# Performance work log

Measured on AMD Instinct MI355X. Metric: run time of the kernel, lower is better.

## Reference

```python
import jax, jax.numpy as jnp
import numpy as np

EPS = 1e-5

def conv_bn(x, w, bn):
    # 1x1 conv (no bias) + BatchNorm2d in eval mode.
    # x: [B,C,H,W], w: [O,C], bn: [4,O] = (gamma, beta, running_mean, running_var)
    y = jnp.einsum('bchw,oc->bohw', x, w)
    g, b, m, v = bn[0], bn[1], bn[2], bn[3]
    s = g * jax.lax.rsqrt(v + EPS)
    return y * s[None, :, None, None] + (b - m * s)[None, :, None, None]

def setup_inputs() -> dict:
    key = jax.random.key(0)
    ks = jax.random.split(key, 10)
    dim, nh_kd, dh = 384, 256, 1024
    return {
        'x':   jax.random.normal(ks[0], (16, dim, 32, 32), dtype=jnp.float32),
        'wq':  jax.random.normal(ks[1], (nh_kd, dim), dtype=jnp.float32) * 0.05,
        'bnq': jax.random.uniform(ks[2], (4, nh_kd), dtype=jnp.float32),
        'wk':  jax.random.normal(ks[3], (nh_kd, dim), dtype=jnp.float32) * 0.05,
        'bnk': jax.random.uniform(ks[4], (4, nh_kd), dtype=jnp.float32),
        'wv':  jax.random.normal(ks[5], (dh, dim), dtype=jnp.float32) * 0.05,
        'bnv': jax.random.uniform(ks[6], (4, dh), dtype=jnp.float32),
        'wp':  jax.random.normal(ks[7], (dim, dh), dtype=jnp.float32) * 0.05,
        'bnp': jax.random.uniform(ks[8], (4, dim), dtype=jnp.float32),
        'num_heads': 8,
    }

def reference(x, wq, bnq, wk, bnk, wv, bnv, wp, bnp, num_heads):
    B, C, H, W = x.shape
    N = H * W
    nh = num_heads
    kd = wq.shape[0] // nh          # key_dim
    d = wv.shape[0] // nh           # attn_ratio * key_dim
    dh = wv.shape[0]
    scale = kd ** (-0.5)

    qq = conv_bn(x, wq, bnq).reshape(B, nh, kd, N).transpose(0, 1, 3, 2)  # [B,nh,N,kd]
    kk = conv_bn(x, wk, bnk).reshape(B, nh, kd, N)                         # [B,nh,kd,N]
    vv = conv_bn(x, wv, bnv).reshape(B, nh, d, N).transpose(0, 1, 3, 2)    # [B,nh,N,d]

    # NOTE: original divides by scale (i.e. multiplies by sqrt(key_dim)); kept faithfully.
    attn = jnp.einsum('bhnk,bhkm->bhnm', qq, kk) / scale
    attn = jax.nn.softmax(attn, axis=-1)
    xx = jnp.einsum('bhnm,bhmd->bhnd', attn, vv)           # [B,nh,N,d]
    xx = xx.transpose(0, 1, 3, 2).reshape(B, dh, H, W)
    return conv_bn(xx, wp, bnp)
```

## Files before the change

### kernel.cpp

```cpp
#include <hip/hip_runtime.h>

typedef _Float16 f16x8 __attribute__((ext_vector_type(8)));
typedef _Float16 f16x4 __attribute__((ext_vector_type(4)));
typedef __fp16 h16x2 __attribute__((ext_vector_type(2)));
typedef float f32x4 __attribute__((ext_vector_type(4)));
typedef float f32x16 __attribute__((ext_vector_type(16)));

#define BN_EPS 1e-5f
#define SQRT32 5.656854249492381f
#define LOG2E  1.4426950408889634f

typedef const __attribute__((address_space(1))) void* gas_p;
typedef __attribute__((address_space(3))) void* las_p;

__global__ __launch_bounds__(256) void prep(
    const float* __restrict__ x,
    const float* __restrict__ wq, const float* __restrict__ wk,
    const float* __restrict__ wv, const float* __restrict__ wp,
    const float* __restrict__ bnq, const float* __restrict__ bnk,
    const float* __restrict__ bnv, const float* __restrict__ bnp,
    _Float16* __restrict__ xT_hi, _Float16* __restrict__ xT_lo,
    _Float16* __restrict__ wqk_h, _Float16* __restrict__ wqk_l,
    _Float16* __restrict__ wv_h,  _Float16* __restrict__ wp_h,
    float* __restrict__ s_qkv, float* __restrict__ t_qkv,
    float* __restrict__ s_p,   float* __restrict__ t_p)
{
    __shared__ float Tx[64][65];
    const int t = threadIdx.x;
    if (blockIdx.z < 16) {
        const int ct = blockIdx.x, nt = blockIdx.y, b = blockIdx.z;
        const int c0 = ct * 64, n0 = nt * 64;
        {
            int tr = t >> 4, tc = (t & 15) * 4;
            #pragma unroll
            for (int p = 0; p < 4; p++) {
                int r = tr + p * 16;
                float4 v = *(const float4*)(x + ((size_t)(b * 384 + c0 + r)) * 1024 + n0 + tc);
                Tx[r][tc + 0] = v.x; Tx[r][tc + 1] = v.y; Tx[r][tc + 2] = v.z; Tx[r][tc + 3] = v.w;
            }
        }
        __syncthreads();
        {
            int nn = t >> 2, cc = (t & 3) * 16;
            f16x8 h0, h1, l0, l1;
            #pragma unroll
            for (int i = 0; i < 8; i++) {
                float v = Tx[cc + i][nn];
                _Float16 hh = (_Float16)v;
                h0[i] = hh; l0[i] = (_Float16)(v - (float)hh);
            }
            #pragma unroll
            for (int i = 0; i < 8; i++) {
                float v = Tx[cc + 8 + i][nn];
                _Float16 hh = (_Float16)v;
                h1[i] = hh; l1[i] = (_Float16)(v - (float)hh);
            }
            size_t o = ((size_t)(b * 1024 + n0 + nn)) * 384 + c0 + cc;
            *(f16x8*)(xT_hi + o) = h0; *(f16x8*)(xT_hi + o + 8) = h1;
            *(f16x8*)(xT_lo + o) = l0; *(f16x8*)(xT_lo + o + 8) = l1;
        }
    } else {
        const int NQK = 512 * 384, NV = 1024 * 384, NP = 384 * 1024;
        int tid = (blockIdx.y * 6 + blockIdx.x) * 256 + t;
        for (int i = tid; i < NQK + NV + NP; i += 24576) {
            if (i < NQK) {
                int o = i / 384, c = i - o * 384;
                float v = (o < 256) ? wq[o * 384 + c] : wk[(o - 256) * 384 + c];
                _Float16 hh = (_Float16)v;
                wqk_h[i] = hh; wqk_l[i] = (_Float16)(v - (float)hh);
            } else if (i < NQK + NV) {
                wv_h[i - NQK] = (_Float16)wv[i - NQK];
            } else {
                wp_h[i - NQK - NV] = (_Float16)wp[i - NQK - NV];
            }
        }
        if (tid < 1536) {
            int i = tid;
            float g, be, m, v;
            if (i < 256)      { int o = i;       g = bnq[o]; be = bnq[256 + o];  m = bnq[512 + o];  v = bnq[768 + o]; }
            else if (i < 512) { int o = i - 256; g = bnk[o]; be = bnk[256 + o];  m = bnk[512 + o];  v = bnk[768 + o]; }
            else              { int o = i - 512; g = bnv[o]; be = bnv[1024 + o]; m = bnv[2048 + o]; v = bnv[3072 + o]; }
            float s = g * rsqrtf(v + BN_EPS);
            float tt = be - m * s;
            if (i < 256) { s *= SQRT32 * LOG2E; tt *= SQRT32 * LOG2E; }
            s_qkv[i] = s; t_qkv[i] = tt;
        } else if (tid < 1536 + 384) {
            int o = tid - 1536;
            float g = bnp[o], be = bnp[384 + o], m = bnp[768 + o], v = bnp[1152 + o];
            float s = g * rsqrtf(v + BN_EPS);
            s_p[o] = s; t_p[o] = be - m * s;
        }
    }
}

__global__ __launch_bounds__(256, 2) void gemm_qkv(
    const _Float16* __restrict__ wqk_h, const _Float16* __restrict__ wqk_l,
    const _Float16* __restrict__ wv_h,
    const _Float16* __restrict__ xT_hi, const _Float16* __restrict__ xT_lo,
    const float* __restrict__ S, const float* __restrict__ T,
    _Float16* __restrict__ qT_h, _Float16* __restrict__ qT_l,
    _Float16* __restrict__ kT_h, _Float16* __restrict__ kT_l,
    _Float16* __restrict__ vbuf)
{
    __shared__ __align__(16) _Float16 As_h[128 * 40];
    __shared__ __align__(16) _Float16 As_l[128 * 40];
    __shared__ __align__(16) _Float16 Bs_h[128 * 40];
    __shared__ __align__(16) _Float16 Bs_l[128 * 40];
    const int t = threadIdx.x, lane = t & 63, w = t >> 6;
    const int wr = w >> 1, wc = w & 1, l16 = lane & 15, lq = lane >> 4;
    const int bx = blockIdx.x, n0 = blockIdx.y * 128, b = blockIdx.z;
    const bool isv = bx >= 4;
    const int o0 = isv ? (bx - 4) * 128 : bx * 128;
    const _Float16* __restrict__ Ah = isv ? wv_h : wqk_h;

    f32x4 acc[4][4] = {};

    for (int kb = 0; kb < 384; kb += 32) {
        __syncthreads();
        #pragma unroll
        for (int p = 0; p < 2; p++) {
            int g = t + p * 256, row = g >> 2, ch = g & 3;
            *(uint4*)(&As_h[row * 40 + ch * 8]) =
                *(const uint4*)(Ah + (size_t)(o0 + row) * 384 + kb + ch * 8);
        }
        #pragma unroll
        for (int p = 0; p < 2; p++) {
            int g = t + p * 256, row = g >> 2, ch = g & 3;
            *(uint4*)(&Bs_h[row * 40 + ch * 8]) =
                *(const uint4*)(xT_hi + ((size_t)(b * 1024) + n0 + row) * 384 + kb + ch * 8);
        }
        if (!isv) {
            #pragma unroll
            for (int p = 0; p < 2; p++) {
                int g = t + p * 256, row = g >> 2, ch = g & 3;
                *(uint4*)(&As_l[row * 40 + ch * 8]) =
                    *(const uint4*)(wqk_l + (size_t)(o0 + row) * 384 + kb + ch * 8);
            }
            #pragma unroll
            for (int p = 0; p < 2; p++) {
                int g = t + p * 256, row = g >> 2, ch = g & 3;
                *(uint4*)(&Bs_l[row * 40 + ch * 8]) =
                    *(const uint4*)(xT_lo + ((size_t)(b * 1024) + n0 + row) * 384 + kb + ch * 8);
            }
        }
        __syncthreads();

        if (!isv) {
            f16x8 ah[4], al[4], bh[4], bl[4];
            #pragma unroll
            for (int i = 0; i < 4; i++) {
                ah[i] = *(const f16x8*)(&Bs_h[(wr * 64 + i * 16 + l16) * 40 + lq * 8]);
                al[i] = *(const f16x8*)(&Bs_l[(wr * 64 + i * 16 + l16) * 40 + lq * 8]);
            }
            #pragma unroll
            for (int j = 0; j < 4; j++) {
                bh[j] = *(const f16x8*)(&As_h[(wc * 64 + j * 16 + l16) * 40 + lq * 8]);
                bl[j] = *(const f16x8*)(&As_l[(wc * 64 + j * 16 + l16) * 40 + lq * 8]);
            }
            #pragma unroll
            for (int i = 0; i < 4; i++)
                #pragma unroll
                for (int j = 0; j < 4; j++) {
                    acc[i][j] = __builtin_amdgcn_mfma_f32_16x16x32_f16(ah[i], bh[j], acc[i][j], 0, 0, 0);
                    acc[i][j] = __builtin_amdgcn_mfma_f32_16x16x32_f16(al[i], bh[j], acc[i][j], 0, 0, 0);
                    acc[i][j] = __builtin_amdgcn_mfma_f32_16x16x32_f16(ah[i], bl[j], acc[i][j], 0, 0, 0);
                }
        } else {
            f16x8 a[4], bf[4];
            #pragma unroll
            for (int i = 0; i < 4; i++) a[i]  = *(const f16x8*)(&As_h[(wr * 64 + i * 16 + l16) * 40 + lq * 8]);
            #pragma unroll
            for (int j = 0; j < 4; j++) bf[j] = *(const f16x8*)(&Bs_h[(wc * 64 + j * 16 + l16) * 40 + lq * 8]);
            #pragma unroll
            for (int i = 0; i < 4; i++)
                #pragma unroll
                for (int j = 0; j < 4; j++)
                    acc[i][j] = __builtin_amdgcn_mfma_f32_16x16x32_f16(a[i], bf[j], acc[i][j], 0, 0, 0);
        }
    }

    if (!isv) {
        #pragma unroll
        for (int i = 0; i < 4; i++) {
            #pragma unroll
            for (int r = 0; r < 4; r++) {
                int n = n0 + wr * 64 + i * 16 + lq * 4 + r;
                #pragma unroll
                for (int j = 0; j < 4; j++) {
                    int o = o0 + wc * 64 + j * 16 + l16;
                    float sc = S[o], sh = T[o];
                    float v = acc[i][j][r] * sc + sh;
                    _Float16 hh = (_Float16)v;
                    _Float16 ll = (_Float16)(v - (float)hh);
                    if (o < 256) {
                        size_t idx = (((size_t)(b * 8) + (o >> 5)) * 1024 + n) * 32 + (o & 31);
                        qT_h[idx] = hh; qT_l[idx] = ll;
                    } else {
                        int oo = o - 256;
                        int hd = oo >> 5, c = oo & 31;
                        int f = ((n >> 5) & 1) * 2 + (c >> 4);
                        size_t idx = ((((size_t)(b * 8 + hd) * 16 + (n >> 6)) * 4 + f) * 64
                                      + ((c >> 3) & 1) * 32 + (n & 31)) * 8 + (c & 7);
                        kT_h[idx] = hh; kT_l[idx] = ll;
                    }
                }
            }
        }
    } else {
        #pragma unroll
        for (int i = 0; i < 4; i++) {
            #pragma unroll
            for (int r = 0; r < 4; r++) {
                int o = o0 + wr * 64 + i * 16 + lq * 4 + r;
                float sc = S[512 + o], sh = T[512 + o];
                #pragma unroll
                for (int j = 0; j < 4; j++) {
                    int n = n0 + wc * 64 + j * 16 + l16;
                    int k = n & 63;
                    int s4 = k >> 4, c4 = (k >> 2) & 3;
                    int ep = s4 * 16 + (c4 & 1) * 8 + (c4 >> 1) * 4 + (k & 3);
                    int nst = (n & ~63) | ep;
                    vbuf[((size_t)(b * 1024) + o) * 1024 + nst] = (_Float16)(acc[i][j][r] * sc + sh);
                }
            }
        }
    }
}

__device__ __forceinline__ f32x16 qk6(f16x8 kh0, f16x8 kl0, f16x8 kh1, f16x8 kl1,
                                      f16x8 qh0, f16x8 ql0, f16x8 qh1, f16x8 ql1) {
    f32x16 c = {};
    c = __builtin_amdgcn_mfma_f32_32x32x16_f16(kh0, qh0, c, 0, 0, 0);
    c = __builtin_amdgcn_mfma_f32_32x32x16_f16(kl0, qh0, c, 0, 0, 0);
    c = __builtin_amdgcn_mfma_f32_32x32x16_f16(kh0, ql0, c, 0, 0, 0);
    c = __builtin_amdgcn_mfma_f32_32x32x16_f16(kh1, qh1, c, 0, 0, 0);
    c = __builtin_amdgcn_mfma_f32_32x32x16_f16(kl1, qh1, c, 0, 0, 0);
    c = __builtin_amdgcn_mfma_f32_32x32x16_f16(kh1, ql1, c, 0, 0, 0);
    return c;
}

__global__ __launch_bounds__(256, 3) void attn(
    const _Float16* __restrict__ qT_h, const _Float16* __restrict__ qT_l,
    const _Float16* __restrict__ kT_h, const _Float16* __restrict__ kT_l,
    const _Float16* __restrict__ vbuf,
    _Float16* __restrict__ xxT_h, _Float16* __restrict__ xxT_l)
{
    __shared__ __align__(16) _Float16 Vs[2][128 * 64];
    __shared__ __align__(16) _Float16 Ksh[2][2048];
    __shared__ __align__(16) _Float16 Ksl[2][2048];
    const int t = threadIdx.x, lane = t & 63, w = t >> 6;
    const int L = lane & 31, hl = lane >> 5;
    const int bh = blockIdx.x, qt = blockIdx.y;
    const int b = bh >> 3, h = bh & 7;
    const size_t vbase = ((size_t)(b * 1024) + h * 128) * 1024;

    f16x8 bq_h[2], bq_l[2];
    {
        int q = qt * 128 + w * 32 + L;
        #pragma unroll
        for (int kh = 0; kh < 2; kh++) {
            size_t base = ((size_t)(bh * 1024) + q) * 32 + kh * 16 + hl * 8;
            bq_h[kh] = *(const f16x8*)(qT_h + base);
            bq_l[kh] = *(const f16x8*)(qT_l + base);
        }
    }

    f32x16 o_acc[4] = {};
    float m_st = -INFINITY, l_st = 0.f;

    #define DMA_TILE(buf, kt_)                                                     \
        {                                                                          \
            size_t ktb = (size_t)(bh * 16 + (kt_)) * 2048 + (size_t)t * 8;         \
            __builtin_amdgcn_global_load_lds((gas_p)(const void*)(kT_h + ktb),     \
                                             (las_p)(void*)&Ksh[buf][w * 512], 16, 0, 0); \
            __builtin_amdgcn_global_load_lds((gas_p)(const void*)(kT_l + ktb),     \
                                             (las_p)(void*)&Ksl[buf][w * 512], 16, 0, 0); \
            _Pragma("unroll")                                                      \
            for (int p = 0; p < 4; p++) {                                          \
                int g2 = t + p * 256;                                              \
                int d = g2 >> 3;                                                   \
                int kcg = (g2 & 7) ^ (d & 7);                                      \
                const _Float16* src = vbuf + vbase + (size_t)d * 1024              \
                                      + (kt_) * 64 + kcg * 8;                      \
                _Float16* dst = &Vs[buf][(p * 256 + w * 64) * 8];                  \
                __builtin_amdgcn_global_load_lds((gas_p)(const void*)src,          \
                                                 (las_p)(void*)dst, 16, 0, 0);     \
            }                                                                      \
        }

    DMA_TILE(0, 0)
    __syncthreads();

    for (int kt = 0; kt < 16; kt++) {
        const int cur = kt & 1;

        if (kt < 15) DMA_TILE(cur ^ 1, kt + 1)

        const _Float16* khp = &Ksh[cur][lane * 8];
        const _Float16* klp = &Ksl[cur][lane * 8];
        f16x8 K0h = *(const f16x8*)(khp);
        f16x8 K1h = *(const f16x8*)(khp + 512);
        f16x8 K2h = *(const f16x8*)(khp + 1024);
        f16x8 K3h = *(const f16x8*)(khp + 1536);
        f16x8 K0l = *(const f16x8*)(klp);
        f16x8 K1l = *(const f16x8*)(klp + 512);
        f16x8 K2l = *(const f16x8*)(klp + 1024);
        f16x8 K3l = *(const f16x8*)(klp + 1536);

        __builtin_amdgcn_s_setprio(1);
        f32x16 c0 = qk6(K0h, K0l, K1h, K1l, bq_h[0], bq_l[0], bq_h[1], bq_l[1]);
        f32x16 c1 = qk6(K2h, K2l, K3h, K3l, bq_h[0], bq_l[0], bq_h[1], bq_l[1]);
        __builtin_amdgcn_s_setprio(0);

        float tmx[16];
        #pragma unroll
        for (int i = 0; i < 16; i++) tmx[i] = fmaxf(c0[i], c1[i]);
        #pragma unroll
        for (int st = 8; st >= 1; st >>= 1)
            #pragma unroll
            for (int i = 0; i < st; i++) tmx[i] = fmaxf(tmx[i], tmx[i + st]);
        float mx = fmaxf(tmx[0], __shfl_xor(tmx[0], 32, 64));

        if (__any(mx > m_st + 8.f)) {
            float mnew = fmaxf(m_st, mx);
            float a = exp2f(m_st - mnew);
            l_st *= a;
            #pragma unroll
            for (int dt = 0; dt < 4; dt++)
                #pragma unroll
                for (int i = 0; i < 16; i++) o_acc[dt][i] *= a;
            m_st = mnew;
        }

        f16x8 pf[4];
        float rs = 0.f;
        #pragma unroll
        for (int s = 0; s < 4; s++) {
            float pv[8];
            #pragma unroll
            for (int j = 0; j < 8; j++) {
                float cv = (s < 2) ? c0[(s & 1) * 8 + j] : c1[(s & 1) * 8 + j];
                pv[j] = exp2f(cv - m_st);
            }
            rs += ((pv[0] + pv[1]) + (pv[2] + pv[3])) + ((pv[4] + pv[5]) + (pv[6] + pv[7]));
            union { f16x8 v; h16x2 h[4]; } u;
            #pragma unroll
            for (int j = 0; j < 4; j++)
                u.h[j] = __builtin_amdgcn_cvt_pkrtz(pv[2 * j], pv[2 * j + 1]);
            pf[s] = u.v;
        }
        l_st += rs;

        __builtin_amdgcn_s_setprio(1);
        #pragma unroll
        for (int s = 0; s < 4; s++) {
            #pragma unroll
            for (int dt = 0; dt < 4; dt++) {
                int cp = (2 * s + hl) ^ (L & 7);
                f16x8 avp = *(const f16x8*)(&Vs[cur][(dt * 32 + L) * 64 + cp * 8]);
                o_acc[dt] = __builtin_amdgcn_mfma_f32_32x32x16_f16(avp, pf[s], o_acc[dt], 0, 0, 0);
            }
        }
        __builtin_amdgcn_s_setprio(0);

        if (kt < 15) __syncthreads();
    }
    #undef DMA_TILE

    l_st += __shfl_xor(l_st, 32, 64);

    {
        float rl = 1.f / l_st;
        int q = qt * 128 + w * 32 + L;
        #pragma unroll
        for (int dt = 0; dt < 4; dt++) {
            #pragma unroll
            for (int gg = 0; gg < 4; gg++) {
                f16x4 hv, lv;
                #pragma unroll
                for (int rr = 0; rr < 4; rr++) {
                    float v = o_acc[dt][gg * 4 + rr] * rl;
                    _Float16 hh = (_Float16)v;
                    hv[rr] = hh; lv[rr] = (_Float16)(v - (float)hh);
                }
                size_t o = ((size_t)(b * 1024) + q) * 1024 + h * 128 + dt * 32 + gg * 8 + hl * 4;
                *(f16x4*)(xxT_h + o) = hv;
                *(f16x4*)(xxT_l + o) = lv;
            }
        }
    }
}

__global__ __launch_bounds__(256, 2) void gemm_out(
    const _Float16* __restrict__ wp_h,
    const _Float16* __restrict__ xxT_h, const _Float16* __restrict__ xxT_l,
    const float* __restrict__ S, const float* __restrict__ T,
    float* __restrict__ out)
{
    __shared__ __align__(16) _Float16 As[128 * 40];
    __shared__ __align__(16) _Float16 Bh[64 * 40];
    __shared__ __align__(16) _Float16 Bl[64 * 40];
    const int t = threadIdx.x, lane = t & 63, w = t >> 6;
    const int wr = w >> 1, wc = w & 1, l16 = lane & 15, lq = lane >> 4;
    const int o0 = blockIdx.x * 128, n0 = blockIdx.y * 64, b = blockIdx.z;

    f32x4 acc[4][2] = {};

    for (int kb = 0; kb < 1024; kb += 32) {
        __syncthreads();
        #pragma unroll
        for (int p = 0; p < 2; p++) {
            int g = t + p * 256, row = g >> 2, ch = g & 3;
            *(uint4*)(&As[row * 40 + ch * 8]) =
                *(const uint4*)(wp_h + (size_t)(o0 + row) * 1024 + kb + ch * 8);
        }
        {
            int row = t >> 2, ch = t & 3;
            size_t src = ((size_t)(b * 1024) + n0 + row) * 1024 + kb + ch * 8;
            *(uint4*)(&Bh[row * 40 + ch * 8]) = *(const uint4*)(xxT_h + src);
            *(uint4*)(&Bl[row * 40 + ch * 8]) = *(const uint4*)(xxT_l + src);
        }
        __syncthreads();

        f16x8 a[4], bh[2], bl[2];
        #pragma unroll
        for (int i = 0; i < 4; i++) a[i] = *(const f16x8*)(&As[(wr * 64 + i * 16 + l16) * 40 + lq * 8]);
        #pragma unroll
        for (int j = 0; j < 2; j++) {
            bh[j] = *(const f16x8*)(&Bh[(wc * 32 + j * 16 + l16) * 40 + lq * 8]);
            bl[j] = *(const f16x8*)(&Bl[(wc * 32 + j * 16 + l16) * 40 + lq * 8]);
        }
        #pragma unroll
        for (int i = 0; i < 4; i++)
            #pragma unroll
            for (int j = 0; j < 2; j++) {
                acc[i][j] = __builtin_amdgcn_mfma_f32_16x16x32_f16(a[i], bh[j], acc[i][j], 0, 0, 0);
                acc[i][j] = __builtin_amdgcn_mfma_f32_16x16x32_f16(a[i], bl[j], acc[i][j], 0, 0, 0);
            }
    }

    #pragma unroll
    for (int i = 0; i < 4; i++) {
        #pragma unroll
        for (int r = 0; r < 4; r++) {
            int o = o0 + wr * 64 + i * 16 + lq * 4 + r;
            float sc = S[o], sh = T[o];
            #pragma unroll
            for (int j = 0; j < 2; j++) {
                int n = n0 + wc * 32 + j * 16 + l16;
                out[((size_t)(b * 384) + o) * 1024 + n] = acc[i][j][r] * sc + sh;
            }
        }
    }
}


extern "C" void kernel_launch(void* const* d_in, const int* in_sizes, int n_in,
                              void* d_out, int out_size, void* d_ws, size_t ws_size,
                              hipStream_t stream) {
    const float* x   = (const float*)d_in[0];
    const float* wq  = (const float*)d_in[1];
    const float* bnq = (const float*)d_in[2];
    const float* wk  = (const float*)d_in[3];
    const float* bnk = (const float*)d_in[4];
    const float* wv  = (const float*)d_in[5];
    const float* bnv = (const float*)d_in[6];
    const float* wp  = (const float*)d_in[7];
    const float* bnp = (const float*)d_in[8];
    float* out = (float*)d_out;
    (void)in_sizes; (void)n_in; (void)out_size; (void)ws_size;

    char* ws = (char*)d_ws;
    size_t off = 0;
    auto alloc = [&](size_t bytes) {
        void* p = ws + off;
        off = (off + bytes + 255) & ~(size_t)255;
        return p;
    };
    _Float16* xT_hi = (_Float16*)alloc((size_t)16 * 1024 * 384 * 2);
    _Float16* xT_lo = (_Float16*)alloc((size_t)16 * 1024 * 384 * 2);
    _Float16* wqk_h = (_Float16*)alloc((size_t)512 * 384 * 2);
    _Float16* wqk_l = (_Float16*)alloc((size_t)512 * 384 * 2);
    _Float16* wv_h  = (_Float16*)alloc((size_t)1024 * 384 * 2);
    alloc((size_t)7 * 1024 * 1024);
    _Float16* xxT_h = (_Float16*)d_ws;
    _Float16* wp_h  = (_Float16*)alloc((size_t)384 * 1024 * 2);
    float*    s_qkv = (float*)alloc(1536 * 4);
    float*    t_qkv = (float*)alloc(1536 * 4);
    float*    s_p   = (float*)alloc(384 * 4);
    float*    t_p   = (float*)alloc(384 * 4);
    _Float16* qT_h  = (_Float16*)alloc((size_t)16 * 8 * 1024 * 32 * 2);
    _Float16* qT_l  = (_Float16*)alloc((size_t)16 * 8 * 1024 * 32 * 2);
    _Float16* kT_h  = (_Float16*)alloc((size_t)16 * 8 * 1024 * 32 * 2);
    _Float16* kT_l  = (_Float16*)alloc((size_t)16 * 8 * 1024 * 32 * 2);
    _Float16* vbuf  = (_Float16*)alloc((size_t)16 * 1024 * 1024 * 2);
    _Float16* xxT_l = (_Float16*)alloc((size_t)16 * 1024 * 1024 * 2);

    prep<<<dim3(6, 16, 17), dim3(256), 0, stream>>>(
        x, wq, wk, wv, wp, bnq, bnk, bnv, bnp,
        xT_hi, xT_lo, wqk_h, wqk_l, wv_h, wp_h, s_qkv, t_qkv, s_p, t_p);

    gemm_qkv<<<dim3(12, 8, 16), dim3(256), 0, stream>>>(
        wqk_h, wqk_l, wv_h, xT_hi, xT_lo, s_qkv, t_qkv,
        qT_h, qT_l, kT_h, kT_l, vbuf);

    attn<<<dim3(128, 8), dim3(256), 0, stream>>>(qT_h, qT_l, kT_h, kT_l, vbuf, xxT_h, xxT_l);

    gemm_out<<<dim3(3, 16, 16), dim3(256), 0, stream>>>(wp_h, xxT_h, xxT_l, s_p, t_p, out);
}
```

Before: 308.4 us.

## Software-pipeline attention PV MFMAs one tile behind softmax using triple-buffered V

The P·V MFMA step for tile kt-1 now runs inside iteration kt, interleaved with the softmax of tile kt. V tiles are triple-buffered in LDS so the previous tile's V stays resident while the next one is loaded by DMA. The row-max reduction is also reshaped into a shallower tree of 3-input max operations. The aim is to overlap exp/max VALU work with matrix-core work. In exchange, LDS use grows and the occupancy hint drops from 3 to 2 blocks per CU, which may reduce latency hiding.

```diff
diff --git a/kernel.cpp b/kernel.cpp
--- a/kernel.cpp
+++ b/kernel.cpp
@@ -239,13 +239,13 @@
     return c;
 }
 
-__global__ __launch_bounds__(256, 3) void attn(
+__global__ __launch_bounds__(256, 2) void attn(
     const _Float16* __restrict__ qT_h, const _Float16* __restrict__ qT_l,
     const _Float16* __restrict__ kT_h, const _Float16* __restrict__ kT_l,
     const _Float16* __restrict__ vbuf,
     _Float16* __restrict__ xxT_h, _Float16* __restrict__ xxT_l)
 {
-    __shared__ __align__(16) _Float16 Vs[2][128 * 64];
+    __shared__ __align__(16) _Float16 Vs[3][128 * 64];
     __shared__ __align__(16) _Float16 Ksh[2][2048];
     __shared__ __align__(16) _Float16 Ksl[2][2048];
     const int t = threadIdx.x, lane = t & 63, w = t >> 6;
@@ -267,14 +267,15 @@
 
     f32x16 o_acc[4] = {};
     float m_st = -INFINITY, l_st = 0.f;
-
-    #define DMA_TILE(buf, kt_)                                                     \
+    f16x8 pf[4];
+
+    #define DMA_TILE(vb, kb, kt_)                                                  \
         {                                                                          \
             size_t ktb = (size_t)(bh * 16 + (kt_)) * 2048 + (size_t)t * 8;         \
             __builtin_amdgcn_global_load_lds((gas_p)(const void*)(kT_h + ktb),     \
-                                             (las_p)(void*)&Ksh[buf][w * 512], 16, 0, 0); \
+                                             (las_p)(void*)&Ksh[kb][w * 512], 16, 0, 0); \
             __builtin_amdgcn_global_load_lds((gas_p)(const void*)(kT_l + ktb),     \
-                                             (las_p)(void*)&Ksl[buf][w * 512], 16, 0, 0); \
+                                             (las_p)(void*)&Ksl[kb][w * 512], 16, 0, 0); \
             _Pragma("unroll")                                                      \
             for (int p = 0; p < 4; p++) {                                          \
                 int g2 = t + p * 256;                                              \
@@ -282,22 +283,23 @@
                 int kcg = (g2 & 7) ^ (d & 7);                                      \
                 const _Float16* src = vbuf + vbase + (size_t)d * 1024              \
                                       + (kt_) * 64 + kcg * 8;                      \
-                _Float16* dst = &Vs[buf][(p * 256 + w * 64) * 8];                  \
+                _Float16* dst = &Vs[vb][(p * 256 + w * 64) * 8];                   \
                 __builtin_amdgcn_global_load_lds((gas_p)(const void*)src,          \
                                                  (las_p)(void*)dst, 16, 0, 0);     \
             }                                                                      \
         }
 
-    DMA_TILE(0, 0)
+    DMA_TILE(0, 0, 0)
     __syncthreads();
 
     for (int kt = 0; kt < 16; kt++) {
-        const int cur = kt & 1;
-
-        if (kt < 15) DMA_TILE(cur ^ 1, kt + 1)
-
-        const _Float16* khp = &Ksh[cur][lane * 8];
-        const _Float16* klp = &Ksl[cur][lane * 8];
+        const int kcur = kt & 1;
+        const int vprv = (kt + 2) % 3;
+
+        if (kt < 15) DMA_TILE((kt + 1) % 3, kcur ^ 1, kt + 1)
+
+        const _Float16* khp = &Ksh[kcur][lane * 8];
+        const _Float16* klp = &Ksl[kcur][lane * 8];
         f16x8 K0h = *(const f16x8*)(khp);
         f16x8 K1h = *(const f16x8*)(khp + 512);
         f16x8 K2h = *(const f16x8*)(khp + 1024);
@@ -312,14 +314,33 @@
         f32x16 c1 = qk6(K2h, K2l, K3h, K3l, bq_h[0], bq_l[0], bq_h[1], bq_l[1]);
         __builtin_amdgcn_s_setprio(0);
 
-        float tmx[16];
-        #pragma unroll
-        for (int i = 0; i < 16; i++) tmx[i] = fmaxf(c0[i], c1[i]);
-        #pragma unroll
-        for (int st = 8; st >= 1; st >>= 1)
-            #pragma unroll
-            for (int i = 0; i < st; i++) tmx[i] = fmaxf(tmx[i], tmx[i + st]);
-        float mx = fmaxf(tmx[0], __shfl_xor(tmx[0], 32, 64));
+        if (kt) {
+            __builtin_amdgcn_s_setprio(1);
+            #pragma unroll
+            for (int s = 0; s < 4; s++) {
+                int cp = (2 * s + hl) ^ (L & 7);
+                #pragma unroll
+                for (int dt = 0; dt < 4; dt++) {
+                    f16x8 avp = *(const f16x8*)(&Vs[vprv][(dt * 32 + L) * 64 + cp * 8]);
+                    o_acc[dt] = __builtin_amdgcn_mfma_f32_32x32x16_f16(avp, pf[s], o_acc[dt], 0, 0, 0);
+                }
+            }
+            __builtin_amdgcn_s_setprio(0);
+        }
+
+        #define EL(e) ((e) < 16 ? c0[e] : c1[(e) - 16])
+        float t1[11];
+        #pragma unroll
+        for (int g = 0; g < 10; g++)
+            t1[g] = fmaxf(fmaxf(EL(3 * g), EL(3 * g + 1)), EL(3 * g + 2));
+        t1[10] = fmaxf(EL(30), EL(31));
+        #undef EL
+        float t2a = fmaxf(fmaxf(t1[0], t1[1]), t1[2]);
+        float t2b = fmaxf(fmaxf(t1[3], t1[4]), t1[5]);
+        float t2c = fmaxf(fmaxf(t1[6], t1[7]), t1[8]);
+        float t2d = fmaxf(t1[9], t1[10]);
+        float mx0 = fmaxf(fmaxf(t2a, t2b), fmaxf(t2c, t2d));
+        float mx = fmaxf(mx0, __shfl_xor(mx0, 32, 64));
 
         if (__any(mx > m_st + 8.f)) {
             float mnew = fmaxf(m_st, mx);
@@ -332,7 +353,6 @@
             m_st = mnew;
         }
 
-        f16x8 pf[4];
         float rs = 0.f;
         #pragma unroll
         for (int s = 0; s < 4; s++) {
@@ -343,29 +363,31 @@
                 pv[j] = exp2f(cv - m_st);
             }
             rs += ((pv[0] + pv[1]) + (pv[2] + pv[3])) + ((pv[4] + pv[5]) + (pv[6] + pv[7]));
-            union { f16x8 v; h16x2 h[4]; } u;
+            union { f16x8 v; h16x2 hh[4]; } u;
             #pragma unroll
             for (int j = 0; j < 4; j++)
-                u.h[j] = __builtin_amdgcn_cvt_pkrtz(pv[2 * j], pv[2 * j + 1]);
+                u.hh[j] = __builtin_amdgcn_cvt_pkrtz(pv[2 * j], pv[2 * j + 1]);
             pf[s] = u.v;
         }
         l_st += rs;
 
+        if (kt < 15) __syncthreads();
+    }
+    #undef DMA_TILE
+
+    {
         __builtin_amdgcn_s_setprio(1);
         #pragma unroll
         for (int s = 0; s < 4; s++) {
+            int cp = (2 * s + hl) ^ (L & 7);
             #pragma unroll
             for (int dt = 0; dt < 4; dt++) {
-                int cp = (2 * s + hl) ^ (L & 7);
-                f16x8 avp = *(const f16x8*)(&Vs[cur][(dt * 32 + L) * 64 + cp * 8]);
+                f16x8 avp = *(const f16x8*)(&Vs[0][(dt * 32 + L) * 64 + cp * 8]);
                 o_acc[dt] = __builtin_amdgcn_mfma_f32_32x32x16_f16(avp, pf[s], o_acc[dt], 0, 0, 0);
             }
         }
         __builtin_amdgcn_s_setprio(0);
-
-        if (kt < 15) __syncthreads();
-    }
-    #undef DMA_TILE
+    }
 
     l_st += __shfl_xor(l_st, 32, 64);
 
```

Result: no change. 307.2 us (-0.4%).
